# Optimization experiments

Measured on AMD Instinct MI355X. Metric: run time of the kernel, lower is better.

The kernel has to match this reference:

```python
import jax, jax.numpy as jnp
import numpy as np

B, N, P, C, H = 8, 512, 16, 512, 8
HD = C // H  # 64


def setup_inputs() -> dict:
    key = jax.random.key(0)
    k1, k2, k3, k4, k5 = jax.random.split(key, 5)
    x = jax.random.normal(k1, (B, N, P, C), dtype=jnp.float32)
    # binary observation mask; force slot 0 valid so masked mean never divides by 0
    mask = (jax.random.uniform(k2, (B, N, P)) > 0.3).astype(jnp.float32)
    mask = mask.at[:, :, 0].set(1.0)
    lens = jax.random.randint(k3, (B,), 1, N)
    lens_mask = jnp.ones((B, N), dtype=jnp.float32)
    # parameters (torch Linear stored as [in, out] here; qkv_bias=False, proj has bias)
    Wqkv = jax.random.normal(k4, (C, 3 * C), dtype=jnp.float32) * (1.0 / np.sqrt(C))
    Wproj = jax.random.normal(k5, (C, C), dtype=jnp.float32) * (1.0 / np.sqrt(C))
    bproj = jnp.zeros((C,), dtype=jnp.float32)
    return {"x": x, "mask": mask, "lens": lens, "lens_mask": lens_mask,
            "Wqkv": Wqkv, "Wproj": Wproj, "bproj": bproj}


def reference(x, mask, lens, lens_mask, Wqkv, Wproj, bproj):
    # lens / lens_mask are unused by the original forward
    b, n, p, c = x.shape
    h, hd = H, c // H
    qkv = jnp.einsum('bnpc,cd->bnpd', x, Wqkv).reshape(b, n, p, 3, h, hd)
    # q: take P-slot 0                       -> [B,H,N,hd]
    q = qkv[:, :, 0, 0].transpose(0, 2, 1, 3)
    # k: masked mean over P                  -> [B,H,N,hd]
    m = mask[..., None, None]                      # [B,N,P,1,1]
    k = (jnp.where(m > 0, qkv[:, :, :, 1], 0.0).sum(axis=2) / m.sum(axis=2))
    k = k.transpose(0, 2, 1, 3)
    # v: pack P into channel dim             -> [B,H,N,hd*P]
    v = qkv[:, :, :, 2].transpose(0, 3, 1, 4, 2).reshape(b, h, n, hd * p)
    # SDPA over N (scale by 1/sqrt(head_dim of q))
    scale = 1.0 / np.sqrt(hd)
    attn = jax.nn.softmax(jnp.einsum('bhnd,bhmd->bhnm', q, k) * scale, axis=-1)
    out = jnp.einsum('bhnm,bhme->bhne', attn, v)            # [B,H,N,hd*P]
    # unpack P back out                       -> [B,N,P,C]
    out = out.reshape(b, h, n, hd, p).transpose(0, 2, 4, 1, 3).reshape(b, n, p, c)
    return out @ Wproj + bproj
```

## Files before the change

kernel.cpp:

```cpp
#include <hip/hip_runtime.h>

typedef _Float16 f16;
typedef __attribute__((ext_vector_type(8))) _Float16 half8;
typedef __attribute__((ext_vector_type(2))) _Float16 half2v;
typedef __attribute__((ext_vector_type(4))) float float4v;

#define MODE_QK 0
#define MODE_V 1
#define MODE_PV 2
#define MODE_PROJ 3


__device__ __forceinline__ void gload16(const f16* g, f16* l) {
    __builtin_amdgcn_global_load_lds(
        (const __attribute__((address_space(1))) void*)g,
        (__attribute__((address_space(3))) void*)l, 16, 0, 0);
}

__global__ __launch_bounds__(256) void prep_kernel(
    const float* __restrict__ x, const float* __restrict__ mask,
    const float* __restrict__ Wqkv, const float* __restrict__ Wproj,
    f16* __restrict__ xf, f16* __restrict__ xmean,
    f16* __restrict__ WT, f16* __restrict__ WpT)
{
    if (blockIdx.x >= 4096) {
        int idx = (blockIdx.x - 4096) * 256 + threadIdx.x;
        if (idx < 1536 * 512) {
            int d = idx >> 9, c = idx & 511;
            WT[idx] = (f16)Wqkv[c * 1536 + d];
        } else {
            int i2 = idx - 1536 * 512;
            int d = i2 >> 9, c = i2 & 511;
            WpT[i2] = (f16)Wproj[c * 512 + d];
        }
        return;
    }
    int bn = blockIdx.x;
    int t = threadIdx.x;
    const float* xrow = x + (size_t)bn * 16 * 512;
    const float* mrow = mask + (size_t)bn * 16;
    float msum = 0.f;
    #pragma unroll
    for (int p = 0; p < 16; p++) msum += mrow[p];
    int c = t * 2;
    float a0 = 0.f, a1 = 0.f;
    #pragma unroll
    for (int p = 0; p < 16; p++) {
        float2 v = *(const float2*)(xrow + p * 512 + c);
        float m = mrow[p];
        a0 += m * v.x; a1 += m * v.y;
        half2v h; h[0] = (f16)v.x; h[1] = (f16)v.y;
        *(half2v*)(xf + (size_t)bn * 16 * 512 + p * 512 + c) = h;
    }
    float inv = 1.f / msum;
    half2v hm; hm[0] = (f16)(a0 * inv); hm[1] = (f16)(a1 * inv);
    *(half2v*)(xmean + (size_t)bn * 512 + c) = hm;
}

template<int MODE>
__global__ __launch_bounds__(256) void gemm128(
    const f16* __restrict__ pA, const f16* __restrict__ pA2,
    const f16* __restrict__ pB,
    f16* __restrict__ outa, f16* __restrict__ outb,
    float* __restrict__ outf, const float* __restrict__ bias)
{
    __shared__ __align__(16) f16 sm[8192];
    f16* As = sm;
    f16* Bs = sm + 4096;
    const int t = threadIdx.x;
    const int lane = t & 63;
    const int w = t >> 6;
    const int wm = w & 1, wn = w >> 1;
    const int quad = lane >> 4, l15 = lane & 15;

    const int n0 = blockIdx.x * 128;
    const int m0 = blockIdx.y * 128;
    int vb = 0, vp = 0, z = 0;

    const f16* Abase; size_t sA;
    const f16* Bbase; size_t sB;
    if constexpr (MODE == MODE_QK) {
        if (n0 < 512) { Abase = pA;  sA = 8192; }
        else          { Abase = pA2; sA = 512;  }
        Bbase = pB; sB = 512;
    } else if constexpr (MODE == MODE_V) {
        z = blockIdx.z; vb = z >> 4; vp = z & 15;
        Abase = pA; sA = 512;
        Bbase = pB + ((size_t)vb * 512 * 16 + vp) * 512; sB = 8192;
    } else if constexpr (MODE == MODE_PV) {
        z = blockIdx.z;
        Abase = pA + (size_t)z * 512 * 512; sA = 512;
        Bbase = pB + (size_t)z * 1024 * 512; sB = 512;
    } else {
        Abase = pA; sA = 512;
        Bbase = pB; sB = 512;
    }

    const int rlo = (lane >> 2), kof = (lane & 3) * 8;
    const f16* ga0 = Abase + (size_t)(m0 + w * 16 + rlo) * sA + kof;
    const f16* ga1 = Abase + (size_t)(m0 + (w + 4) * 16 + rlo) * sA + kof;
    const f16* gb0 = Bbase + (size_t)(n0 + w * 16 + rlo) * sB + kof;
    const f16* gb1 = Bbase + (size_t)(n0 + (w + 4) * 16 + rlo) * sB + kof;
    f16* lA0 = As + w * 512;
    f16* lA1 = As + (w + 4) * 512;
    f16* lB0 = Bs + w * 512;
    f16* lB1 = Bs + (w + 4) * 512;

    float4v acc[4][4];
    #pragma unroll
    for (int i = 0; i < 4; i++)
        #pragma unroll
        for (int j = 0; j < 4; j++)
            acc[i][j] = (float4v){0.f, 0.f, 0.f, 0.f};

    for (int kt = 0; kt < 16; kt++) {
        __syncthreads();
        gload16(ga0, lA0); gload16(ga1, lA1);
        gload16(gb0, lB0); gload16(gb1, lB1);
        ga0 += 32; ga1 += 32; gb0 += 32; gb1 += 32;
        __syncthreads();
        half8 af[4], bf[4];
        #pragma unroll
        for (int mi = 0; mi < 4; mi++)
            af[mi] = *(const half8*)&As[(wm * 64 + mi * 16 + l15) * 32 + quad * 8];
        #pragma unroll
        for (int ni = 0; ni < 4; ni++)
            bf[ni] = *(const half8*)&Bs[(wn * 64 + ni * 16 + l15) * 32 + quad * 8];
        #pragma unroll
        for (int mi = 0; mi < 4; mi++)
            #pragma unroll
            for (int ni = 0; ni < 4; ni++)
                acc[mi][ni] = __builtin_amdgcn_mfma_f32_16x16x32_f16(
                    af[mi], bf[ni], acc[mi][ni], 0, 0, 0);
    }

    __syncthreads();

    if constexpr (MODE == MODE_PROJ) {
        float* pf = (float*)sm;
        const int rp = t >> 4, cp = (t & 15) * 8;
        float4v bb0 = *(const float4v*)&bias[n0 + cp];
        float4v bb1 = *(const float4v*)&bias[n0 + cp + 4];
        #pragma unroll
        for (int ci = 0; ci < 8; ci++) {
            if (wm == (ci >> 2)) {
                int mi = ci & 3;
                #pragma unroll
                for (int ni = 0; ni < 4; ni++)
                    #pragma unroll
                    for (int i = 0; i < 4; i++)
                        pf[(quad * 4 + i) * 132 + wn * 64 + ni * 16 + l15] =
                            acc[mi][ni][i];
            }
            __syncthreads();
            float4v v0 = *(const float4v*)&pf[rp * 132 + cp];
            float4v v1 = *(const float4v*)&pf[rp * 132 + cp + 4];
            size_t gb = (size_t)(m0 + ci * 16 + rp) * 512 + n0 + cp;
            *(float4v*)&outf[gb] = v0 + bb0;
            *(float4v*)&outf[gb + 4] = v1 + bb1;
            __syncthreads();
        }
    } else {
        f16* ph = sm;
        const int rp = t >> 3, cp = (t & 7) * 16;
        #pragma unroll
        for (int ci = 0; ci < 4; ci++) {
            if (wm == (ci >> 1)) {
                #pragma unroll
                for (int mh = 0; mh < 2; mh++) {
                    int mi = (ci & 1) * 2 + mh;
                    #pragma unroll
                    for (int ni = 0; ni < 4; ni++)
                        #pragma unroll
                        for (int i = 0; i < 4; i++)
                            ph[(mh * 16 + quad * 4 + i) * 136 + wn * 64 + ni * 16 + l15] =
                                (f16)acc[mi][ni][i];
                }
            }
            __syncthreads();
            int gr = m0 + ci * 32 + rp;
            #pragma unroll
            for (int s = 0; s < 2; s++) {
                half8 v = *(const half8*)&ph[rp * 136 + cp + s * 8];
                int gc = n0 + cp + s * 8;
                if constexpr (MODE == MODE_QK) {
                    int b = gr >> 9, n = gr & 511;
                    if (gc < 512)
                        *(half8*)&outa[(((size_t)(b * 8 + (gc >> 6))) * 512 + n) * 64 + (gc & 63)] = v;
                    else {
                        int jj = gc - 512;
                        *(half8*)&outb[(((size_t)(b * 8 + (jj >> 6))) * 512 + n) * 64 + (jj & 63)] = v;
                    }
                } else if constexpr (MODE == MODE_V) {
                    int h = gr >> 6, dd = gr & 63;
                    *(half8*)&outa[(((size_t)(vb * 8 + h)) * 1024 + vp * 64 + dd) * 512 + gc] = v;
                } else {
                    int p = gc >> 6, dd = gc & 63;
                    int b = z >> 3, h = z & 7;
                    *(half8*)&outa[((size_t)(b * 512 + gr) * 16 + p) * 512 + h * 64 + dd] = v;
                }
            }
            __syncthreads();
        }
    }
}

__global__ __launch_bounds__(256) void qk_softmax_kernel(
    const f16* __restrict__ q, const f16* __restrict__ k, f16* __restrict__ Pout)
{
    __shared__ __align__(16) f16 sm[16896];
    const int t = threadIdx.x;
    const int lane = t & 63, w = t >> 6;
    const int quad = lane >> 4, l15 = lane & 15;
    const int bh = blockIdx.y;
    const int n0 = blockIdx.x * 64;

    const f16* kbase = k + (size_t)bh * 512 * 64;
    const f16* qp = q + ((size_t)bh * 512 + n0 + w * 16 + l15) * 64 + quad * 8;
    half8 a0 = *(const half8*)qp;
    half8 a1 = *(const half8*)(qp + 32);

    float4v acc[32];
    #pragma unroll
    for (int f = 0; f < 32; f++) acc[f] = (float4v){0.f, 0.f, 0.f, 0.f};

    const int srow = lane >> 3, scol = lane & 7;
    #pragma unroll
    for (int c = 0; c < 4; c++) {
        __syncthreads();
        #pragma unroll
        for (int i = 0; i < 4; i++) {
            int ci2 = w * 4 + i;
            int row = ci2 * 8 + srow;
            gload16(kbase + c * 8192 + row * 64 + ((scol ^ (row & 7)) << 3),
                    sm + ci2 * 512 + lane * 8);
        }
        __syncthreads();
        #pragma unroll
        for (int fl = 0; fl < 8; fl++) {
            int row16 = fl * 16 + l15;
            int sw = row16 & 7;
            half8 b0 = *(const half8*)&sm[row16 * 64 + ((quad ^ sw) << 3)];
            half8 b1 = *(const half8*)&sm[row16 * 64 + (((quad + 4) ^ sw) << 3)];
            acc[c * 8 + fl] = __builtin_amdgcn_mfma_f32_16x16x32_f16(
                a0, b0, acc[c * 8 + fl], 0, 0, 0);
            acc[c * 8 + fl] = __builtin_amdgcn_mfma_f32_16x16x32_f16(
                a1, b1, acc[c * 8 + fl], 0, 0, 0);
        }
    }

    float mx0 = -3e38f, mx1 = -3e38f, mx2 = -3e38f, mx3 = -3e38f;
    #pragma unroll
    for (int f = 0; f < 32; f++) {
        mx0 = fmaxf(mx0, acc[f][0]); mx1 = fmaxf(mx1, acc[f][1]);
        mx2 = fmaxf(mx2, acc[f][2]); mx3 = fmaxf(mx3, acc[f][3]);
    }
    #pragma unroll
    for (int off = 1; off < 16; off <<= 1) {
        mx0 = fmaxf(mx0, __shfl_xor(mx0, off));
        mx1 = fmaxf(mx1, __shfl_xor(mx1, off));
        mx2 = fmaxf(mx2, __shfl_xor(mx2, off));
        mx3 = fmaxf(mx3, __shfl_xor(mx3, off));
    }
    float s0 = 0.f, s1 = 0.f, s2 = 0.f, s3 = 0.f;
    #pragma unroll
    for (int f = 0; f < 32; f++) {
        float e0 = __expf(0.125f * (acc[f][0] - mx0));
        float e1 = __expf(0.125f * (acc[f][1] - mx1));
        float e2 = __expf(0.125f * (acc[f][2] - mx2));
        float e3 = __expf(0.125f * (acc[f][3] - mx3));
        acc[f][0] = e0; acc[f][1] = e1; acc[f][2] = e2; acc[f][3] = e3;
        s0 += e0; s1 += e1; s2 += e2; s3 += e3;
    }
    #pragma unroll
    for (int off = 1; off < 16; off <<= 1) {
        s0 += __shfl_xor(s0, off);
        s1 += __shfl_xor(s1, off);
        s2 += __shfl_xor(s2, off);
        s3 += __shfl_xor(s3, off);
    }
    float r0 = 1.f / s0, r1 = 1.f / s1, r2 = 1.f / s2, r3 = 1.f / s3;

    __syncthreads();
    f16* pb = sm + w * 4224;
    const int rr = lane >> 2, cb = (lane & 3) * 64;
    #pragma unroll
    for (int cc = 0; cc < 2; cc++) {
        #pragma unroll
        for (int ff = 0; ff < 16; ff++) {
            int f = cc * 16 + ff;
            pb[(quad * 4 + 0) * 264 + ff * 16 + l15] = (f16)(acc[f][0] * r0);
            pb[(quad * 4 + 1) * 264 + ff * 16 + l15] = (f16)(acc[f][1] * r1);
            pb[(quad * 4 + 2) * 264 + ff * 16 + l15] = (f16)(acc[f][2] * r2);
            pb[(quad * 4 + 3) * 264 + ff * 16 + l15] = (f16)(acc[f][3] * r3);
        }
        size_t gb = ((size_t)bh * 512 + n0 + w * 16 + rr) * 512 + cc * 256 + cb;
        #pragma unroll
        for (int s = 0; s < 8; s++) {
            half8 v = *(const half8*)&pb[rr * 264 + cb + s * 8];
            *(half8*)&Pout[gb + s * 8] = v;
        }
    }
}

extern "C" void kernel_launch(void* const* d_in, const int* in_sizes, int n_in,
                              void* d_out, int out_size, void* d_ws, size_t ws_size,
                              hipStream_t stream)
{
    (void)in_sizes; (void)n_in; (void)out_size; (void)ws_size;
    const float* x     = (const float*)d_in[0];
    const float* mask  = (const float*)d_in[1];
    const float* Wqkv  = (const float*)d_in[4];
    const float* Wproj = (const float*)d_in[5];
    const float* bproj = (const float*)d_in[6];
    float* out = (float*)d_out;
    char* ws = (char*)d_ws;

    f16* xf16  = (f16*)(ws + 0);
    f16* vT    = (f16*)(ws + 67108864);
    f16* xmean = (f16*)(ws + 134217728);
    f16* WT    = (f16*)(ws + 138412032);
    f16* WpT   = (f16*)(ws + 139984896);
    f16* qb    = (f16*)(ws + 140509184);
    f16* kb    = (f16*)(ws + 144703488);
    f16* Pm    = (f16*)(ws + 148897792);
    f16* ypre  = xf16;

    prep_kernel<<<dim3(8192), dim3(256), 0, stream>>>(
        x, mask, Wqkv, Wproj, xf16, xmean, WT, WpT);
    gemm128<MODE_QK><<<dim3(8, 32), dim3(256), 0, stream>>>(
        xf16, xmean, WT, qb, kb, nullptr, nullptr);
    gemm128<MODE_V><<<dim3(4, 4, 128), dim3(256), 0, stream>>>(
        WT + 1024 * 512, nullptr, xf16, vT, nullptr, nullptr, nullptr);
    qk_softmax_kernel<<<dim3(8, 64), dim3(256), 0, stream>>>(qb, kb, Pm);
    gemm128<MODE_PV><<<dim3(8, 4, 64), dim3(256), 0, stream>>>(
        Pm, nullptr, vT, ypre, nullptr, nullptr, nullptr);
    gemm128<MODE_PROJ><<<dim3(4, 512), dim3(256), 0, stream>>>(
        ypre, nullptr, WpT, nullptr, nullptr, out, bproj);
}
```

Measured before the change: 467.4 us.

## Double-buffer GEMM LDS tiles and use per-wave epilogue staging

The 128x128 GEMM now uses two LDS buffers. The next K-tile's global-to-LDS load is issued before computing on the current one, which removes one barrier per iteration and overlaps load latency with MFMA work. The epilogue gives each wave its own LDS staging region, so block-wide __syncthreads between output chunks are no longer needed. LDS use grows from 16KB to 36KB per block, which may reduce occupancy.

New measurement: 438.6 us. -6.2%, faster.

```diff
diff --git a/kernel.cpp b/kernel.cpp
--- a/kernel.cpp
+++ b/kernel.cpp
@@ -64,9 +64,7 @@
     f16* __restrict__ outa, f16* __restrict__ outb,
     float* __restrict__ outf, const float* __restrict__ bias)
 {
-    __shared__ __align__(16) f16 sm[8192];
-    f16* As = sm;
-    f16* Bs = sm + 4096;
+    __shared__ __align__(16) f16 sm[18432];
     const int t = threadIdx.x;
     const int lane = t & 63;
     const int w = t >> 6;
@@ -101,10 +99,6 @@
     const f16* ga1 = Abase + (size_t)(m0 + (w + 4) * 16 + rlo) * sA + kof;
     const f16* gb0 = Bbase + (size_t)(n0 + w * 16 + rlo) * sB + kof;
     const f16* gb1 = Bbase + (size_t)(n0 + (w + 4) * 16 + rlo) * sB + kof;
-    f16* lA0 = As + w * 512;
-    f16* lA1 = As + (w + 4) * 512;
-    f16* lB0 = Bs + w * 512;
-    f16* lB1 = Bs + (w + 4) * 512;
 
     float4v acc[4][4];
     #pragma unroll
@@ -113,94 +107,98 @@
         for (int j = 0; j < 4; j++)
             acc[i][j] = (float4v){0.f, 0.f, 0.f, 0.f};
 
+    {
+        f16* d = sm;
+        gload16(ga0, d + w * 512); gload16(ga1, d + (w + 4) * 512);
+        gload16(gb0, d + 4096 + w * 512); gload16(gb1, d + 4096 + (w + 4) * 512);
+        ga0 += 32; ga1 += 32; gb0 += 32; gb1 += 32;
+    }
+    int cur = 0;
     for (int kt = 0; kt < 16; kt++) {
         __syncthreads();
-        gload16(ga0, lA0); gload16(ga1, lA1);
-        gload16(gb0, lB0); gload16(gb1, lB1);
-        ga0 += 32; ga1 += 32; gb0 += 32; gb1 += 32;
-        __syncthreads();
+        if (kt < 15) {
+            f16* d = sm + (cur ^ 1) * 8192;
+            gload16(ga0, d + w * 512); gload16(ga1, d + (w + 4) * 512);
+            gload16(gb0, d + 4096 + w * 512); gload16(gb1, d + 4096 + (w + 4) * 512);
+            ga0 += 32; ga1 += 32; gb0 += 32; gb1 += 32;
+        }
+        const f16* Asr = sm + cur * 8192;
+        const f16* Bsr = Asr + 4096;
         half8 af[4], bf[4];
         #pragma unroll
         for (int mi = 0; mi < 4; mi++)
-            af[mi] = *(const half8*)&As[(wm * 64 + mi * 16 + l15) * 32 + quad * 8];
+            af[mi] = *(const half8*)&Asr[(wm * 64 + mi * 16 + l15) * 32 + quad * 8];
         #pragma unroll
         for (int ni = 0; ni < 4; ni++)
-            bf[ni] = *(const half8*)&Bs[(wn * 64 + ni * 16 + l15) * 32 + quad * 8];
+            bf[ni] = *(const half8*)&Bsr[(wn * 64 + ni * 16 + l15) * 32 + quad * 8];
         #pragma unroll
         for (int mi = 0; mi < 4; mi++)
             #pragma unroll
             for (int ni = 0; ni < 4; ni++)
                 acc[mi][ni] = __builtin_amdgcn_mfma_f32_16x16x32_f16(
                     af[mi], bf[ni], acc[mi][ni], 0, 0, 0);
+        cur ^= 1;
     }
 
     __syncthreads();
 
     if constexpr (MODE == MODE_PROJ) {
-        float* pf = (float*)sm;
-        const int rp = t >> 4, cp = (t & 15) * 8;
-        float4v bb0 = *(const float4v*)&bias[n0 + cp];
-        float4v bb1 = *(const float4v*)&bias[n0 + cp + 4];
-        #pragma unroll
-        for (int ci = 0; ci < 8; ci++) {
-            if (wm == (ci >> 2)) {
-                int mi = ci & 3;
+        float* pwf = (float*)sm + w * 2176;
+        const int rr4 = lane >> 4, c4 = (lane & 15) * 4;
+        float4v bb = *(const float4v*)&bias[n0 + wn * 64 + c4];
+        #pragma unroll
+        for (int c2 = 0; c2 < 2; c2++) {
+            #pragma unroll
+            for (int mh = 0; mh < 2; mh++) {
+                int mi = c2 * 2 + mh;
                 #pragma unroll
                 for (int ni = 0; ni < 4; ni++)
                     #pragma unroll
                     for (int i = 0; i < 4; i++)
-                        pf[(quad * 4 + i) * 132 + wn * 64 + ni * 16 + l15] =
+                        pwf[(mh * 16 + quad * 4 + i) * 68 + ni * 16 + l15] =
                             acc[mi][ni][i];
             }
-            __syncthreads();
-            float4v v0 = *(const float4v*)&pf[rp * 132 + cp];
-            float4v v1 = *(const float4v*)&pf[rp * 132 + cp + 4];
-            size_t gb = (size_t)(m0 + ci * 16 + rp) * 512 + n0 + cp;
-            *(float4v*)&outf[gb] = v0 + bb0;
-            *(float4v*)&outf[gb + 4] = v1 + bb1;
-            __syncthreads();
+            #pragma unroll
+            for (int s = 0; s < 8; s++) {
+                int r = s * 4 + rr4;
+                float4v v = *(const float4v*)&pwf[r * 68 + c4];
+                *(float4v*)&outf[(size_t)(m0 + wm * 64 + c2 * 32 + r) * 512 +
+                                 n0 + wn * 64 + c4] = v + bb;
+            }
         }
     } else {
-        f16* ph = sm;
-        const int rp = t >> 3, cp = (t & 7) * 16;
-        #pragma unroll
-        for (int ci = 0; ci < 4; ci++) {
-            if (wm == (ci >> 1)) {
+        f16* pw = sm + w * 4608;
+        #pragma unroll
+        for (int mi = 0; mi < 4; mi++)
+            #pragma unroll
+            for (int ni = 0; ni < 4; ni++)
                 #pragma unroll
-                for (int mh = 0; mh < 2; mh++) {
-                    int mi = (ci & 1) * 2 + mh;
-                    #pragma unroll
-                    for (int ni = 0; ni < 4; ni++)
-                        #pragma unroll
-                        for (int i = 0; i < 4; i++)
-                            ph[(mh * 16 + quad * 4 + i) * 136 + wn * 64 + ni * 16 + l15] =
-                                (f16)acc[mi][ni][i];
+                for (int i = 0; i < 4; i++)
+                    pw[(mi * 16 + quad * 4 + i) * 72 + ni * 16 + l15] =
+                        (f16)acc[mi][ni][i];
+        const int rr8 = lane >> 3, c8 = (lane & 7) * 8;
+        #pragma unroll
+        for (int s = 0; s < 8; s++) {
+            int r = s * 8 + rr8;
+            half8 v = *(const half8*)&pw[r * 72 + c8];
+            int gr = m0 + wm * 64 + r;
+            int gc = n0 + wn * 64 + c8;
+            if constexpr (MODE == MODE_QK) {
+                int b = gr >> 9, n = gr & 511;
+                if (gc < 512)
+                    *(half8*)&outa[(((size_t)(b * 8 + (gc >> 6))) * 512 + n) * 64 + (gc & 63)] = v;
+                else {
+                    int jj = gc - 512;
+                    *(half8*)&outb[(((size_t)(b * 8 + (jj >> 6))) * 512 + n) * 64 + (jj & 63)] = v;
                 }
+            } else if constexpr (MODE == MODE_V) {
+                int h = gr >> 6, dd = gr & 63;
+                *(half8*)&outa[(((size_t)(vb * 8 + h)) * 1024 + vp * 64 + dd) * 512 + gc] = v;
+            } else {
+                int p = gc >> 6, dd = gc & 63;
+                int b = z >> 3, h = z & 7;
+                *(half8*)&outa[((size_t)(b * 512 + gr) * 16 + p) * 512 + h * 64 + dd] = v;
             }
-            __syncthreads();
-            int gr = m0 + ci * 32 + rp;
-            #pragma unroll
-            for (int s = 0; s < 2; s++) {
-                half8 v = *(const half8*)&ph[rp * 136 + cp + s * 8];
-                int gc = n0 + cp + s * 8;
-                if constexpr (MODE == MODE_QK) {
-                    int b = gr >> 9, n = gr & 511;
-                    if (gc < 512)
-                        *(half8*)&outa[(((size_t)(b * 8 + (gc >> 6))) * 512 + n) * 64 + (gc & 63)] = v;
-                    else {
-                        int jj = gc - 512;
-                        *(half8*)&outb[(((size_t)(b * 8 + (jj >> 6))) * 512 + n) * 64 + (jj & 63)] = v;
-                    }
-                } else if constexpr (MODE == MODE_V) {
-                    int h = gr >> 6, dd = gr & 63;
-                    *(half8*)&outa[(((size_t)(vb * 8 + h)) * 1024 + vp * 64 + dd) * 512 + gc] = v;
-                } else {
-                    int p = gc >> 6, dd = gc & 63;
-                    int b = z >> 3, h = z & 7;
-                    *(half8*)&outa[((size_t)(b * 512 + gr) * 16 + p) * 512 + h * 64 + dd] = v;
-                }
-            }
-            __syncthreads();
         }
     }
 }
```
